# Kernel optimization log

Measured on AMD Instinct MI355X. Metric: run time of the kernel, lower is better.

The kernel has to match this reference:

```python
import jax, jax.numpy as jnp
from jax import lax
import numpy as np

B, H, W = 2, 48, 48
C_IN, C_OUT = 96, 192
D_INNER, N_STATE, DT_RANK, K = 192, 16, 6, 4  # VMamba: expand=2, d_state=16, dt_rank=ceil(C/16)
EPS = 1e-5


def setup_inputs() -> dict:
    ks = jax.random.split(jax.random.key(0), 16)
    s = 0.02
    r = lambda k, sh, sc=s: jax.random.normal(k, sh, jnp.float32) * sc
    d, N, R = D_INNER, N_STATE, DT_RANK
    return {
        "x": jax.random.normal(ks[0], (B, C_IN, H, W), jnp.float32),
        "ln_g": jnp.ones((C_IN,), jnp.float32),
        "ln_b": jnp.zeros((C_IN,), jnp.float32),
        "in_proj_w": r(ks[1], (2 * d, C_IN)),
        "dwconv_w": r(ks[2], (d, 1, 3, 3)),
        "dwconv_b": jnp.zeros((d,), jnp.float32),
        "x_proj_w": r(ks[3], (K, R + 2 * N, d)),
        "dt_w": r(ks[4], (K, d, R)),
        "dt_b": r(ks[5], (K, d), 0.1),
        "A_logs": jnp.tile(jnp.log(jnp.arange(1, N + 1, dtype=jnp.float32)), (K, d, 1)),
        "Ds": jnp.ones((K, d), jnp.float32),
        "out_norm_g": jnp.ones((d,), jnp.float32),
        "out_norm_b": jnp.zeros((d,), jnp.float32),
        "out_proj_w": r(ks[6], (C_IN, d)),
        "w1": r(ks[7], (C_OUT, C_IN, 1, 1)),
        "b1": jnp.zeros((C_OUT,), jnp.float32),
        "w31": r(ks[8], (C_OUT, C_IN, 3, 3)),
        "b31": jnp.zeros((C_OUT,), jnp.float32),
        "w32": r(ks[9], (C_OUT, C_IN, 3, 3)),
        "b32": jnp.zeros((C_OUT,), jnp.float32),
        "w33": r(ks[10], (C_OUT, C_OUT, 3, 3)),
        "b33": jnp.zeros((C_OUT,), jnp.float32),
        "bn_g": jnp.ones((3 * C_OUT,), jnp.float32),
        "bn_b": jnp.zeros((3 * C_OUT,), jnp.float32),
        "bn_m": r(ks[11], (3 * C_OUT,), 0.1),
        "bn_v": jax.random.uniform(ks[12], (3 * C_OUT,), jnp.float32) + 0.5,
        "prelu_a": jnp.float32(0.25),
    }


def _layernorm(x, g, b):
    m = jnp.mean(x, -1, keepdims=True)
    v = jnp.var(x, -1, keepdims=True)
    return (x - m) * lax.rsqrt(v + EPS) * g + b


def _conv(x, w, b, stride, pad, groups=1):
    y = lax.conv_general_dilated(x, w, (stride, stride), [(pad, pad), (pad, pad)],
                                 dimension_numbers=("NCHW", "OIHW", "NCHW"),
                                 feature_group_count=groups)
    return y + b[None, :, None, None]


def _ss2d(x, in_proj_w, dwconv_w, dwconv_b, x_proj_w, dt_w, dt_b, A_logs, Ds,
          out_norm_g, out_norm_b, out_proj_w):
    # x: (B, H, W, C)
    Bb, Hh, Ww, C = x.shape
    d, N, R = D_INNER, N_STATE, DT_RANK
    L = Hh * Ww
    xz = jnp.einsum("bhwc,ec->bhwe", x, in_proj_w)  # (B,H,W,2d)
    xin, z = jnp.split(xz, 2, axis=-1)
    xc = jnp.transpose(xin, (0, 3, 1, 2))           # (B,d,H,W)
    xc = jax.nn.silu(_conv(xc, dwconv_w, dwconv_b, 1, 1, groups=d))
    # 4 scan directions: row-major, col-major, and their reverses
    x_flat = xc.reshape(Bb, d, L)
    x_t = jnp.transpose(xc, (0, 1, 3, 2)).reshape(Bb, d, L)
    xs = jnp.stack([x_flat, x_t, x_flat[:, :, ::-1], x_t[:, :, ::-1]], axis=1)  # (B,K,d,L)
    x_dbl = jnp.einsum("bkdl,kcd->bkcl", xs, x_proj_w)
    dts, Bs, Cs = x_dbl[:, :, :R], x_dbl[:, :, R:R + N], x_dbl[:, :, R + N:]
    delta = jax.nn.softplus(jnp.einsum("bkrl,kdr->bkdl", dts, dt_w) + dt_b[None, :, :, None])
    A = -jnp.exp(A_logs)                                   # (K,d,N)
    dA = jnp.exp(jnp.einsum("bkdl,kdn->lbkdn", delta, A))  # (L,B,K,d,N)
    dBu = jnp.einsum("bkdl,bknl,bkdl->lbkdn", delta, Bs, xs)
    Cseq = jnp.transpose(Cs, (3, 0, 1, 2))                 # (L,B,K,N)

    def step(h, inp):
        dA_t, dBu_t, c_t = inp
        h = dA_t * h + dBu_t
        return h, jnp.einsum("bkdn,bkn->bkd", h, c_t)

    h0 = jnp.zeros((Bb, K, d, N), x.dtype)
    _, ys = lax.scan(step, h0, (dA, dBu, Cseq))            # ys: (L,B,K,d)
    ys = jnp.transpose(ys, (1, 2, 3, 0)) + xs * Ds[None, :, :, None]  # (B,K,d,L)

    def t_back(a):  # undo the HW transpose of col-major scans
        return jnp.transpose(a.reshape(Bb, d, Ww, Hh), (0, 1, 3, 2)).reshape(Bb, d, L)

    y = ys[:, 0] + ys[:, 2, :, ::-1] + t_back(ys[:, 1]) + t_back(ys[:, 3, :, ::-1])
    y = _layernorm(jnp.transpose(y, (0, 2, 1)), out_norm_g, out_norm_b).reshape(Bb, Hh, Ww, d)
    y = y * jax.nn.silu(z)
    return jnp.einsum("bhwd,cd->bhwc", y, out_proj_w)


def reference(x, ln_g, ln_b, in_proj_w, dwconv_w, dwconv_b, x_proj_w, dt_w, dt_b,
              A_logs, Ds, out_norm_g, out_norm_b, out_proj_w,
              w1, b1, w31, b31, w32, b32, w33, b33,
              bn_g, bn_b, bn_m, bn_v, prelu_a):
    # VSSBlock: residual + SS2D on LayerNorm'd NHWC features
    x_nhwc = jnp.transpose(x, (0, 2, 3, 1))
    x_nhwc = x_nhwc + _ss2d(_layernorm(x_nhwc, ln_g, ln_b), in_proj_w, dwconv_w,
                            dwconv_b, x_proj_w, dt_w, dt_b, A_logs, Ds,
                            out_norm_g, out_norm_b, out_proj_w)
    xm = jnp.transpose(x_nhwc, (0, 3, 1, 2))  # (B,C,H,W)
    # multi-branch stride-2 downsample
    x1 = _conv(xm, w1, b1, 2, 0)
    x2 = _conv(xm, w31, b31, 2, 1)
    x3 = _conv(_conv(xm, w32, b32, 2, 1), w33, b33, 1, 1)
    out = jnp.concatenate([x1, x2, x3], axis=1)  # (B, 3*C_OUT, H/2, W/2)
    # BatchNorm2d (inference, running stats) + PReLU(single param)
    out = (out - bn_m[None, :, None, None]) * lax.rsqrt(bn_v + EPS)[None, :, None, None] \
          * bn_g[None, :, None, None] + bn_b[None, :, None, None]
    return jnp.where(out > 0, out, prelu_a * out)
```

## Files before the change

kernel.cpp:

```cpp
#include <hip/hip_runtime.h>
#include <math.h>

#define BB_ 2
#define HH 48
#define WW 48
#define LL 2304
#define CIN 96
#define DD 192
#define KK 4
#define NN 16
#define RR 6
#define NCH 64
#define LC 36
#define COUT 192
#define OH 24
#define OW 24
#define OHW 576
#define NPX 1152
#define NTOT 4608
#define EPSF 1e-5f

__global__ __launch_bounds__(256) void k_prep(const float* __restrict__ x,
                                              const float* __restrict__ g,
                                              const float* __restrict__ b,
                                              const float* __restrict__ inw,
                                              const float* __restrict__ xpw,
                                              const float* __restrict__ w31,
                                              const float* __restrict__ w32,
                                              const float* __restrict__ w33,
                                              const float* __restrict__ w1,
                                              const float* __restrict__ wout,
                                              float* __restrict__ stats,
                                              float* __restrict__ WgT,
                                              float* __restrict__ sWg,
                                              float* __restrict__ sWb,
                                              float* __restrict__ At3,
                                              float* __restrict__ At1,
                                              float* __restrict__ At2,
                                              float* __restrict__ woutT) {
  __shared__ float tile[32][33];
  int bx = blockIdx.x;
  int tid = threadIdx.x;
  if (bx < 72) {
    int bb = bx / 36; int l0 = (bx % 36) * 64;
    int p = tid >> 2, q = tid & 3;
    int l = l0 + p;
    const float* xp = x + bb * CIN * LL + l;
    float s = 0.f, ss = 0.f;
    for (int c = q; c < CIN; c += 4) { float v = xp[c * LL]; s += v; ss += v * v; }
    s += __shfl_xor(s, 1, 64); s += __shfl_xor(s, 2, 64);
    ss += __shfl_xor(ss, 1, 64); ss += __shfl_xor(ss, 2, 64);
    if (q == 0) {
      float m = s / CIN; float var = ss / CIN - m * m;
      stats[(bb * LL + l) * 2 + 0] = m;
      stats[(bb * LL + l) * 2 + 1] = rsqrtf(var + EPSF);
    }
  } else if (bx == 72) {
    for (int e = tid; e < 2 * DD; e += 256) {
      float swg = 0.f, swb = 0.f;
      for (int c = 0; c < CIN; c++) {
        float w = inw[e * CIN + c];
        float wg = w * g[c];
        WgT[c * 384 + e] = wg;
        swg += wg; swb += w * b[c];
      }
      sWg[e] = swg; sWb[e] = swb;
    }
  } else if (bx < 218) {
    int idx = (bx - 73) * 256 + tid;
    if (idx < 192 * 192) {
      int m = idx % 192, d = idx / 192;
      At3[idx] = (m < 152) ? xpw[m * 192 + d] : 0.f;
    }
  } else if (bx < 542) {
    int tt = bx - 218;
    const float* srcw = (tt < 162) ? w31 : w32;
    int mofs = (tt < 162) ? 0 : 192;
    if (tt >= 162) tt -= 162;
    int kt = tt / 6, mt = tt % 6;
    int r = tid >> 5, c = tid & 31;
    for (int rr = r; rr < 32; rr += 8)
      tile[rr][c] = srcw[(mt * 32 + rr) * 864 + kt * 32 + c];
    __syncthreads();
    for (int rr = r; rr < 32; rr += 8)
      At1[(kt * 32 + rr) * 576 + mofs + mt * 32 + c] = tile[c][rr];
  } else if (bx < 1190) {
    int i = (bx - 542) * 256 + tid;
    if (i < 864 * 192) {
      int k = i / 192, m = i % 192;
      At1[k * 576 + 384 + m] = (k % 9 == 4) ? w1[m * 96 + k / 9] : 0.f;
    }
  } else if (bx < 1514) {
    int tt = bx - 1190;
    int kt = tt / 6, mt = tt % 6;
    int r = tid >> 5, c = tid & 31;
    for (int rr = r; rr < 32; rr += 8)
      tile[rr][c] = w33[(mt * 32 + rr) * 1728 + kt * 32 + c];
    __syncthreads();
    for (int rr = r; rr < 32; rr += 8)
      At2[(kt * 32 + rr) * 192 + mt * 32 + c] = tile[c][rr];
  } else {
    int i = (bx - 1514) * 256 + tid;
    if (i < 192 * 128) {
      int d = i / 128, e = i % 128;
      woutT[i] = (e < 96) ? wout[e * 192 + d] : 0.f;
    }
  }
}

__global__ __launch_bounds__(256) void k_dwconv(const float* __restrict__ xin,
                                                const float* __restrict__ wdw,
                                                const float* __restrict__ bdw,
                                                float* __restrict__ xs,
                                                float* __restrict__ xsl) {
  __shared__ float vt[32 * 50];
  int bid = blockIdx.x;
  int bb = bid / 288; int r = bid % 288; int dg = r / 72; int tile = r % 72;
  int l0 = tile * 32;
  int d0 = dg * 48;
  for (int i = threadIdx.x; i < 32 * 48; i += 256) {
    int lj = i & 31, dl = i >> 5;
    int d = d0 + dl;
    int l = l0 + lj;
    int h = l / WW, w = l % WW;
    const float* xp = xin + (bb * DD + d) * LL;
    const float* wq = wdw + d * 9;
    float acc = bdw[d];
#pragma unroll
    for (int kh = 0; kh < 3; kh++) {
      int ih = h + kh - 1; if (ih < 0 || ih >= HH) continue;
#pragma unroll
      for (int kw = 0; kw < 3; kw++) {
        int iw = w + kw - 1; if (iw < 0 || iw >= WW) continue;
        acc += xp[ih * WW + iw] * wq[kh * 3 + kw];
      }
    }
    float v = acc / (1.f + __expf(-acc));
    vt[lj * 50 + dl] = v;
    xsl[(size_t)d * NTOT + bb * LL + l] = v;
  }
  __syncthreads();
  for (int j = threadIdx.x; j < 32 * 48; j += 256) {
    int lj = j / 48, dl = j - lj * 48;
    int d = d0 + dl;
    int l = l0 + lj;
    int h = l / WW, w = l % WW;
    int lt = w * HH + h;
    float v = vt[lj * 50 + dl];
    xs[((size_t)(bb * 2 + 0) * LL + l) * DD + d] = v;
    xs[((size_t)(bb * 2 + 1) * LL + lt) * DD + d] = v;
  }
}

__global__ __launch_bounds__(256) void k_dtsplit(const float* __restrict__ C1,
                                                 const float* __restrict__ dtw,
                                                 const float* __restrict__ dtb,
                                                 float* __restrict__ Bsb,
                                                 float* __restrict__ Csb,
                                                 float* __restrict__ delta) {
  __shared__ float lds[38 * 33];
  int bid = blockIdx.x;
  int tile = bid % 72; int bk = bid / 72; int bb = bk >> 2; int k = bk & 3;
  int l0 = tile * 32;
  int tid = threadIdx.x;
  for (int i = tid; i < 38 * 32; i += 256) {
    int r = i >> 5, lj = i & 31;
    lds[r * 33 + lj] = C1[(size_t)(k * 38 + r) * NTOT + bb * LL + l0 + lj];
  }
  __syncthreads();
  for (int i = tid; i < 32 * 16; i += 256) {
    int lj = i >> 4, n = i & 15;
    int l = l0 + lj; int h = l / WW, w = l % WW; int lt = w * HH + h;
    int pos = (k == 0) ? l : (k == 1) ? lt : (k == 2) ? (LL - 1 - l) : (LL - 1 - lt);
    size_t base = ((size_t)bk * LL + pos) * NN + n;
    Bsb[base] = lds[(6 + n) * 33 + lj];
    Csb[base] = lds[(22 + n) * 33 + lj];
  }
  for (int i = tid; i < 32 * 192; i += 256) {
    int lj = i / 192, d = i - lj * 192;
    int l = l0 + lj; int h = l / WW, w = l % WW; int lt = w * HH + h;
    int pos = (k == 0) ? l : (k == 1) ? lt : (k == 2) ? (LL - 1 - l) : (LL - 1 - lt);
    const float* wd = dtw + (k * DD + d) * RR;
    float acc = dtb[k * DD + d];
#pragma unroll
    for (int r = 0; r < RR; r++) acc += wd[r] * lds[r * 33 + lj];
    float sp = acc > 20.f ? acc : log1pf(__expf(acc));
    delta[((size_t)bk * LL + pos) * DD + d] = sp;
  }
}

__global__ __launch_bounds__(192) void k_scan1(const float* __restrict__ delta,
                                               const float* __restrict__ xs,
                                               const float* __restrict__ Bsb,
                                               const float* __restrict__ A_logs,
                                               float* __restrict__ Pbuf,
                                               float* __restrict__ Sbuf) {
  __shared__ float Bls[LC * NN];
  int bid = blockIdx.x;
  int c = bid & (NCH - 1); int bk = bid >> 6; int k = bk & 3; int bb = bk >> 2;
  int t0 = c * LC;
  int d = threadIdx.x;
  const float* bp = Bsb + ((size_t)bk * LL + t0) * NN;
  for (int i = d; i < LC * NN; i += 192) Bls[i] = bp[i];
  float A[NN];
  {
    const float4* ap = (const float4*)(A_logs + (k * DD + d) * NN);
#pragma unroll
    for (int j = 0; j < 4; j++) {
      float4 a4 = ap[j];
      A[4 * j + 0] = -__expf(a4.x); A[4 * j + 1] = -__expf(a4.y);
      A[4 * j + 2] = -__expf(a4.z); A[4 * j + 3] = -__expf(a4.w);
    }
  }
  bool seq = true;
#pragma unroll
  for (int n = 0; n < NN; n++) seq = seq && (fabsf(A[n] + (float)(n + 1)) < 1e-3f);
  float h[NN];
#pragma unroll
  for (int n = 0; n < NN; n++) h[n] = 0.f;
  float sd = 0.f;
  __syncthreads();
  const float* dp = delta + ((size_t)bk * LL + t0) * DD + d;
  const float* xpb = xs + ((size_t)(bb * 2 + (k & 1)) * LL) * DD + d;
  const float* xp; int xstep;
  if (k < 2) { xp = xpb + (size_t)t0 * DD; xstep = DD; }
  else       { xp = xpb + (size_t)(LL - 1 - t0) * DD; xstep = -DD; }
#pragma unroll 2
  for (int t = 0; t < LC; ++t) {
    float dt = dp[t * DD];
    float xv = xp[t * xstep];
    float u = dt * xv;
    sd += dt;
    float dA[NN];
    if (seq) {
      float q = __expf(-dt);
      dA[0] = q;
#pragma unroll
      for (int n = 1; n < NN; n++) dA[n] = dA[n - 1] * q;
    } else {
#pragma unroll
      for (int n = 0; n < NN; n++) dA[n] = __expf(dt * A[n]);
    }
    const float4* b4 = (const float4*)&Bls[t * NN];
#pragma unroll
    for (int j = 0; j < 4; j++) {
      float4 bv = b4[j];
      h[4 * j + 0] = dA[4 * j + 0] * h[4 * j + 0] + u * bv.x;
      h[4 * j + 1] = dA[4 * j + 1] * h[4 * j + 1] + u * bv.y;
      h[4 * j + 2] = dA[4 * j + 2] * h[4 * j + 2] + u * bv.z;
      h[4 * j + 3] = dA[4 * j + 3] * h[4 * j + 3] + u * bv.w;
    }
  }
  int chn = (bk * DD + d) * NN;
  float* pp = Pbuf + (size_t)c * 24576 + chn;
  float* sp = Sbuf + (size_t)c * 24576 + chn;
#pragma unroll
  for (int n = 0; n < NN; n++) { pp[n] = __expf(A[n] * sd); sp[n] = h[n]; }
}

__global__ __launch_bounds__(256) void k_scan2(const float* __restrict__ Pbuf,
                                               const float* __restrict__ Sbuf,
                                               float* __restrict__ Hinit) {
  int idx = blockIdx.x * 256 + threadIdx.x;
  float h = 0.f;
  for (int c = 0; c < NCH; c++) {
    Hinit[(size_t)c * 24576 + idx] = h;
    h = Pbuf[(size_t)c * 24576 + idx] * h + Sbuf[(size_t)c * 24576 + idx];
  }
}

__global__ __launch_bounds__(192) void k_scan3(const float* __restrict__ delta,
                                               const float* __restrict__ xs,
                                               const float* __restrict__ Bsb,
                                               const float* __restrict__ Csb,
                                               const float* __restrict__ A_logs,
                                               const float* __restrict__ Ds,
                                               const float* __restrict__ Hinit,
                                               float* __restrict__ ys) {
  __shared__ float Bls[LC * NN];
  __shared__ float Cls[LC * NN];
  int bid = blockIdx.x;
  int c = bid & (NCH - 1); int bk = bid >> 6; int k = bk & 3; int bb = bk >> 2;
  int t0 = c * LC;
  int d = threadIdx.x;
  const float* bp = Bsb + ((size_t)bk * LL + t0) * NN;
  const float* cp = Csb + ((size_t)bk * LL + t0) * NN;
  for (int i = d; i < LC * NN; i += 192) { Bls[i] = bp[i]; Cls[i] = cp[i]; }
  float A[NN];
  {
    const float4* ap = (const float4*)(A_logs + (k * DD + d) * NN);
#pragma unroll
    for (int j = 0; j < 4; j++) {
      float4 a4 = ap[j];
      A[4 * j + 0] = -__expf(a4.x); A[4 * j + 1] = -__expf(a4.y);
      A[4 * j + 2] = -__expf(a4.z); A[4 * j + 3] = -__expf(a4.w);
    }
  }
  bool seq = true;
#pragma unroll
  for (int n = 0; n < NN; n++) seq = seq && (fabsf(A[n] + (float)(n + 1)) < 1e-3f);
  float Dv = Ds[k * DD + d];
  float h[NN];
  {
    const float4* hp = (const float4*)(Hinit + (size_t)c * 24576 + (bk * DD + d) * NN);
#pragma unroll
    for (int j = 0; j < 4; j++) {
      float4 h4 = hp[j];
      h[4 * j + 0] = h4.x; h[4 * j + 1] = h4.y;
      h[4 * j + 2] = h4.z; h[4 * j + 3] = h4.w;
    }
  }
  __syncthreads();
  const float* dp = delta + ((size_t)bk * LL + t0) * DD + d;
  const float* xpb = xs + ((size_t)(bb * 2 + (k & 1)) * LL) * DD + d;
  const float* xp; int xstep;
  if (k < 2) { xp = xpb + (size_t)t0 * DD; xstep = DD; }
  else       { xp = xpb + (size_t)(LL - 1 - t0) * DD; xstep = -DD; }
  float* yp = ys + ((size_t)bk * LL + t0) * DD + d;
#pragma unroll 2
  for (int t = 0; t < LC; ++t) {
    float dt = dp[t * DD];
    float xv = xp[t * xstep];
    float u = dt * xv;
    float y = 0.f;
    float dA[NN];
    if (seq) {
      float q = __expf(-dt);
      dA[0] = q;
#pragma unroll
      for (int n = 1; n < NN; n++) dA[n] = dA[n - 1] * q;
    } else {
#pragma unroll
      for (int n = 0; n < NN; n++) dA[n] = __expf(dt * A[n]);
    }
    const float4* b4 = (const float4*)&Bls[t * NN];
    const float4* c4 = (const float4*)&Cls[t * NN];
#pragma unroll
    for (int j = 0; j < 4; j++) {
      float4 bv = b4[j];
      float4 cc = c4[j];
      h[4 * j + 0] = dA[4 * j + 0] * h[4 * j + 0] + u * bv.x;
      h[4 * j + 1] = dA[4 * j + 1] * h[4 * j + 1] + u * bv.y;
      h[4 * j + 2] = dA[4 * j + 2] * h[4 * j + 2] + u * bv.z;
      h[4 * j + 3] = dA[4 * j + 3] * h[4 * j + 3] + u * bv.w;
      y += h[4 * j + 0] * cc.x + h[4 * j + 1] * cc.y
         + h[4 * j + 2] * cc.z + h[4 * j + 3] * cc.w;
    }
    yp[t * DD] = y + Dv * xv;
  }
}

__global__ __launch_bounds__(256) void k_combine(const float* __restrict__ ys,
                                                 const float* __restrict__ z,
                                                 const float* __restrict__ ong,
                                                 const float* __restrict__ onb,
                                                 float* __restrict__ ya) {
  __shared__ float yt[32 * 193];
  int bx = blockIdx.x; int bb = bx / 72; int l0 = (bx % 72) * 32;
  int tid = threadIdx.x;
  for (int i = tid; i < 32 * DD; i += 256) {
    int p = i / DD, d = i - p * DD;
    int l = l0 + p; int h = l / WW, w = l - h * WW;
    int t1 = w * HH + h;
    float v = ys[(((size_t)bb * KK + 0) * LL + l) * DD + d]
            + ys[(((size_t)bb * KK + 1) * LL + t1) * DD + d]
            + ys[(((size_t)bb * KK + 2) * LL + (LL - 1 - l)) * DD + d]
            + ys[(((size_t)bb * KK + 3) * LL + (LL - 1 - t1)) * DD + d];
    yt[p * 193 + d] = v;
  }
  __syncthreads();
  int p = tid >> 3, q = tid & 7;
  int l = l0 + p;
  float s = 0.f, ss = 0.f;
  for (int d = q * 24; d < q * 24 + 24; d++) { float v = yt[p * 193 + d]; s += v; ss += v * v; }
  s += __shfl_xor(s, 1, 64); s += __shfl_xor(s, 2, 64); s += __shfl_xor(s, 4, 64);
  ss += __shfl_xor(ss, 1, 64); ss += __shfl_xor(ss, 2, 64); ss += __shfl_xor(ss, 4, 64);
  float m = s / DD, var = ss / DD - m * m;
  float rr = rsqrtf(var + EPSF);
  const float* zp = z + (bb * LL + l) * DD;
  for (int d = q * 24; d < q * 24 + 24; d++) {
    float v = (yt[p * 193 + d] - m) * rr * ong[d] + onb[d];
    float zv = zp[d];
    yt[p * 193 + d] = v * zv / (1.f + __expf(-zv));
  }
  __syncthreads();
  for (int i = tid; i < 32 * DD; i += 256) {
    int d = i >> 5, p2 = i & 31;
    ya[(bb * DD + d) * LL + l0 + p2] = yt[p2 * 193 + d];
  }
}

template<int MT, int KCHUNK, int NB>
__global__ __launch_bounds__(256) void k_gemm(const float* __restrict__ At,
                                              const float* __restrict__ Bm,
                                              float* __restrict__ Cout) {
  __shared__ float As[16][64];
  __shared__ float Bs[16][64];
  int n0 = blockIdx.x * 64;
  int m0 = blockIdx.y * 64;
  int kz = blockIdx.z;
  int k0 = kz * KCHUNK;
  int tid = threadIdx.x;
  int lr = tid >> 4;
  int lc = (tid & 15) * 4;
  int tm = tid >> 4;
  int tn = tid & 15;
  float acc[4][4] = {};
  for (int ks = 0; ks < KCHUNK; ks += 16) {
    int kg = k0 + ks + lr;
    *(float4*)&As[lr][lc] = *(const float4*)&At[kg * MT + m0 + lc];
    *(float4*)&Bs[lr][lc] = *(const float4*)&Bm[(size_t)kg * NB + n0 + lc];
    __syncthreads();
#pragma unroll
    for (int kk = 0; kk < 16; kk++) {
      float4 a = *(float4*)&As[kk][tm * 4];
      float4 b = *(float4*)&Bs[kk][tn * 4];
      acc[0][0] += a.x * b.x; acc[0][1] += a.x * b.y; acc[0][2] += a.x * b.z; acc[0][3] += a.x * b.w;
      acc[1][0] += a.y * b.x; acc[1][1] += a.y * b.y; acc[1][2] += a.y * b.z; acc[1][3] += a.y * b.w;
      acc[2][0] += a.z * b.x; acc[2][1] += a.z * b.y; acc[2][2] += a.z * b.z; acc[2][3] += a.z * b.w;
      acc[3][0] += a.w * b.x; acc[3][1] += a.w * b.y; acc[3][2] += a.w * b.z; acc[3][3] += a.w * b.w;
    }
    __syncthreads();
  }
  float* cp = Cout + ((size_t)kz * MT + m0) * NB + n0;
#pragma unroll
  for (int i = 0; i < 4; i++) {
    float4 v = {acc[i][0], acc[i][1], acc[i][2], acc[i][3]};
    *(float4*)&cp[(size_t)(tm * 4 + i) * NB + tn * 4] = v;
  }
}

template<int MT, int KCHUNK, int CI, int IH, int STRIDE>
__global__ __launch_bounds__(256) void k_cgemm(const float* __restrict__ At,
                                               const float* __restrict__ SRC,
                                               float* __restrict__ Cout) {
  __shared__ float As[16][64];
  __shared__ float Bs[16][64];
  int n0 = blockIdx.x * 64;
  int m0 = blockIdx.y * 64;
  int kz = blockIdx.z;
  int k0 = kz * KCHUNK;
  int tid = threadIdx.x;
  int lr = tid >> 4;
  int lc = (tid & 15) * 4;
  int tm = tid >> 4;
  int tn = tid & 15;
  int n = n0 + lc;
  int bb = n / OHW;
  int rem = n - bb * OHW;
  int oh = rem / OW, ow0 = rem - oh * OW;
  float acc[4][4] = {};
  for (int ks = 0; ks < KCHUNK; ks += 16) {
    int kg = k0 + ks + lr;
    int ci = kg / 9, r9 = kg - ci * 9;
    int kh = r9 / 3, kw = r9 - kh * 3;
    int ih = STRIDE * oh + kh - 1;
    const float* src = SRC + ((size_t)(bb * CI + ci)) * (IH * IH) + ih * IH;
    float bvv[4];
#pragma unroll
    for (int j = 0; j < 4; j++) {
      int iw = STRIDE * (ow0 + j) + kw - 1;
      bvv[j] = (ih >= 0 && ih < IH && iw >= 0 && iw < IH) ? src[iw] : 0.f;
    }
    float4 bv = {bvv[0], bvv[1], bvv[2], bvv[3]};
    *(float4*)&Bs[lr][lc] = bv;
    *(float4*)&As[lr][lc] = *(const float4*)&At[kg * MT + m0 + lc];
    __syncthreads();
#pragma unroll
    for (int kk = 0; kk < 16; kk++) {
      float4 a = *(float4*)&As[kk][tm * 4];
      float4 b = *(float4*)&Bs[kk][tn * 4];
      acc[0][0] += a.x * b.x; acc[0][1] += a.x * b.y; acc[0][2] += a.x * b.z; acc[0][3] += a.x * b.w;
      acc[1][0] += a.y * b.x; acc[1][1] += a.y * b.y; acc[1][2] += a.y * b.z; acc[1][3] += a.y * b.w;
      acc[2][0] += a.z * b.x; acc[2][1] += a.z * b.y; acc[2][2] += a.z * b.z; acc[2][3] += a.z * b.w;
      acc[3][0] += a.w * b.x; acc[3][1] += a.w * b.y; acc[3][2] += a.w * b.z; acc[3][3] += a.w * b.w;
    }
    __syncthreads();
  }
  float* cp = Cout + ((size_t)kz * MT + m0) * NPX + n0;
#pragma unroll
  for (int i = 0; i < 4; i++) {
    float4 v = {acc[i][0], acc[i][1], acc[i][2], acc[i][3]};
    *(float4*)&cp[(size_t)(tm * 4 + i) * NPX + tn * 4] = v;
  }
}

template<int MT, int KD, int EPI>
__global__ __launch_bounds__(256) void k_gemmF(const float* __restrict__ At,
                                               const float* __restrict__ Bm,
                                               int ldb, int boffB,
                                               float* __restrict__ C0,
                                               int ldc, int boffC,
                                               const float* __restrict__ a0,
                                               const float* __restrict__ a1,
                                               const float* __restrict__ a2,
                                               float* __restrict__ a3) {
  __shared__ float As[16][64];
  __shared__ float Bs[16][64];
  int n0 = blockIdx.x * 64;
  int m0 = blockIdx.y * 64;
  int bb = blockIdx.z;
  const float* B = Bm + (size_t)bb * boffB;
  int tid = threadIdx.x;
  int lr = tid >> 4;
  int lc = (tid & 15) * 4;
  int tm = tid >> 4;
  int tn = tid & 15;
  float acc[4][4] = {};
  for (int ks = 0; ks < KD; ks += 16) {
    *(float4*)&As[lr][lc] = *(const float4*)&At[(ks + lr) * MT + m0 + lc];
    *(float4*)&Bs[lr][lc] = *(const float4*)&B[(size_t)(ks + lr) * ldb + n0 + lc];
    __syncthreads();
#pragma unroll
    for (int kk = 0; kk < 16; kk++) {
      float4 a = *(float4*)&As[kk][tm * 4];
      float4 b = *(float4*)&Bs[kk][tn * 4];
      acc[0][0] += a.x * b.x; acc[0][1] += a.x * b.y; acc[0][2] += a.x * b.z; acc[0][3] += a.x * b.w;
      acc[1][0] += a.y * b.x; acc[1][1] += a.y * b.y; acc[1][2] += a.y * b.z; acc[1][3] += a.y * b.w;
      acc[2][0] += a.z * b.x; acc[2][1] += a.z * b.y; acc[2][2] += a.z * b.z; acc[2][3] += a.z * b.w;
      acc[3][0] += a.w * b.x; acc[3][1] += a.w * b.y; acc[3][2] += a.w * b.z; acc[3][3] += a.w * b.w;
    }
    __syncthreads();
  }
  int n = n0 + tn * 4;
  if (EPI == 2) {
    float m_[4], r_[4];
#pragma unroll
    for (int j = 0; j < 4; j++) {
      m_[j] = a0[((size_t)bb * LL + n + j) * 2];
      r_[j] = a0[((size_t)bb * LL + n + j) * 2 + 1];
    }
#pragma unroll
    for (int i = 0; i < 4; i++) {
      int e = m0 + tm * 4 + i;
      float swg = a1[e], swb = a2[e];
      float v0 = r_[0] * (acc[i][0] - m_[0] * swg) + swb;
      float v1 = r_[1] * (acc[i][1] - m_[1] * swg) + swb;
      float v2 = r_[2] * (acc[i][2] - m_[2] * swg) + swb;
      float v3 = r_[3] * (acc[i][3] - m_[3] * swg) + swb;
      if (e < DD) {
        float4 v = {v0, v1, v2, v3};
        *(float4*)&C0[(size_t)bb * boffC + (size_t)e * ldc + n] = v;
      } else {
        a3[((size_t)bb * LL + n + 0) * DD + (e - DD)] = v0;
        a3[((size_t)bb * LL + n + 1) * DD + (e - DD)] = v1;
        a3[((size_t)bb * LL + n + 2) * DD + (e - DD)] = v2;
        a3[((size_t)bb * LL + n + 3) * DD + (e - DD)] = v3;
      }
    }
  } else {
#pragma unroll
    for (int i = 0; i < 4; i++) {
      int e = m0 + tm * 4 + i;
      if (e < CIN) {
        size_t off = (size_t)bb * boffC + (size_t)e * ldc + n;
        float4 xr = *(const float4*)&a0[off];
        float4 v = {acc[i][0] + xr.x, acc[i][1] + xr.y, acc[i][2] + xr.z, acc[i][3] + xr.w};
        *(float4*)&C0[off] = v;
      }
    }
  }
}

__global__ __launch_bounds__(256) void k_reduce1(const float* __restrict__ Cp1,
                                                 const float* __restrict__ b1,
                                                 const float* __restrict__ b31,
                                                 const float* __restrict__ b32,
                                                 const float* __restrict__ bn_g,
                                                 const float* __restrict__ bn_b,
                                                 const float* __restrict__ bn_m,
                                                 const float* __restrict__ bn_v,
                                                 const float* __restrict__ prelu_a,
                                                 float* __restrict__ out,
                                                 float* __restrict__ t3) {
  int idx = blockIdx.x * 256 + threadIdx.x;
  if (idx >= 576 * NPX) return;
  int m = idx / NPX, n = idx % NPX;
  float s = 0.f;
#pragma unroll
  for (int c = 0; c < 6; c++) s += Cp1[(size_t)c * 576 * NPX + idx];
  int bb = n / OHW, o = n % OHW;
  if (m < 192) {
    s += b31[m];
    int cc = 192 + m;
    float scale = rsqrtf(bn_v[cc] + EPSF) * bn_g[cc];
    float v = s * scale + (bn_b[cc] - bn_m[cc] * scale);
    float a = prelu_a[0];
    out[((size_t)bb * 576 + cc) * OHW + o] = v > 0.f ? v : a * v;
  } else if (m < 384) {
    s += b32[m - 192];
    t3[((size_t)bb * COUT + (m - 192)) * OHW + o] = s;
  } else {
    s += b1[m - 384];
    int cc = m - 384;
    float scale = rsqrtf(bn_v[cc] + EPSF) * bn_g[cc];
    float v = s * scale + (bn_b[cc] - bn_m[cc] * scale);
    float a = prelu_a[0];
    out[((size_t)bb * 576 + cc) * OHW + o] = v > 0.f ? v : a * v;
  }
}

__global__ __launch_bounds__(256) void k_reduce2(const float* __restrict__ Cp2,
                                                 const float* __restrict__ b33,
                                                 const float* __restrict__ bn_g,
                                                 const float* __restrict__ bn_b,
                                                 const float* __restrict__ bn_m,
                                                 const float* __restrict__ bn_v,
                                                 const float* __restrict__ prelu_a,
                                                 float* __restrict__ out) {
  int idx = blockIdx.x * 256 + threadIdx.x;
  if (idx >= 192 * NPX) return;
  int m = idx / NPX, n = idx % NPX;
  float s = b33[m];
#pragma unroll
  for (int c = 0; c < 9; c++) s += Cp2[(size_t)c * 192 * NPX + idx];
  int bb = n / OHW, o = n % OHW;
  int cc = 384 + m;
  float scale = rsqrtf(bn_v[cc] + EPSF) * bn_g[cc];
  float v = s * scale + (bn_b[cc] - bn_m[cc] * scale);
  float a = prelu_a[0];
  out[((size_t)bb * 576 + cc) * OHW + o] = v > 0.f ? v : a * v;
}

extern "C" void kernel_launch(void* const* d_in, const int* in_sizes, int n_in,
                              void* d_out, int out_size, void* d_ws, size_t ws_size,
                              hipStream_t stream) {
  const float* x        = (const float*)d_in[0];
  const float* ln_g     = (const float*)d_in[1];
  const float* ln_b     = (const float*)d_in[2];
  const float* in_proj_w= (const float*)d_in[3];
  const float* dwconv_w = (const float*)d_in[4];
  const float* dwconv_b = (const float*)d_in[5];
  const float* x_proj_w = (const float*)d_in[6];
  const float* dt_w     = (const float*)d_in[7];
  const float* dt_b     = (const float*)d_in[8];
  const float* A_logs   = (const float*)d_in[9];
  const float* Ds       = (const float*)d_in[10];
  const float* out_norm_g = (const float*)d_in[11];
  const float* out_norm_b = (const float*)d_in[12];
  const float* out_proj_w = (const float*)d_in[13];
  const float* w1  = (const float*)d_in[14];
  const float* b1  = (const float*)d_in[15];
  const float* w31 = (const float*)d_in[16];
  const float* b31 = (const float*)d_in[17];
  const float* w32 = (const float*)d_in[18];
  const float* b32 = (const float*)d_in[19];
  const float* w33 = (const float*)d_in[20];
  const float* b33 = (const float*)d_in[21];
  const float* bn_g = (const float*)d_in[22];
  const float* bn_b = (const float*)d_in[23];
  const float* bn_m = (const float*)d_in[24];
  const float* bn_v = (const float*)d_in[25];
  const float* prelu_a = (const float*)d_in[26];

  float* ws = (float*)d_ws;
  float* stats = ws + 0;
  float* WgT   = ws + 16384;
  float* sWg   = ws + 65536;
  float* sWb   = ws + 66048;
  float* At3   = ws + 98304;
  float* At1   = ws + 147456;
  float* At2   = ws + 655360;
  float* woutT = ws + 1048576;
  float* xin   = ws + 2097152;
  float* z     = ws + 3145728;
  float* xs    = ws + 4194304;
  float* xsl   = ws + 8388608;
  float* C1    = ws + 9437184;
  float* delta = ws + 10485760;
  float* Bsb   = ws + 14155776;
  float* Csb   = ws + 14680064;
  float* Pbuf  = ws + 15728640;
  float* Sbuf  = ws + 17301504;
  float* Hinit = ws + 18874368;
  float* ys    = ws + 20971520;
  float* ya    = ws + 25165824;
  float* xm    = ws + 26214400;
  float* t3    = ws + 27262976;
  float* Cp1   = ws + 31457280;
  float* Cp2   = ws + 35651584;
  float* out = (float*)d_out;

  k_prep<<<1610, 256, 0, stream>>>(x, ln_g, ln_b, in_proj_w, x_proj_w,
                                   w31, w32, w33, w1, out_proj_w,
                                   stats, WgT, sWg, sWb, At3, At1, At2, woutT);
  k_gemmF<384, 96, 2><<<dim3(36, 6, 2), 256, 0, stream>>>(
      WgT, x, LL, CIN * LL, xin, LL, DD * LL, stats, sWg, sWb, z);
  k_dwconv<<<576, 256, 0, stream>>>(xin, dwconv_w, dwconv_b, xs, xsl);
  k_gemm<192, 192, NTOT><<<dim3(72, 3, 1), 256, 0, stream>>>(At3, xsl, C1);
  k_dtsplit<<<576, 256, 0, stream>>>(C1, dt_w, dt_b, Bsb, Csb, delta);
  k_scan1<<<512, 192, 0, stream>>>(delta, xs, Bsb, A_logs, Pbuf, Sbuf);
  k_scan2<<<96, 256, 0, stream>>>(Pbuf, Sbuf, Hinit);
  k_scan3<<<512, 192, 0, stream>>>(delta, xs, Bsb, Csb, A_logs, Ds, Hinit, ys);
  k_combine<<<144, 256, 0, stream>>>(ys, z, out_norm_g, out_norm_b, ya);
  k_gemmF<128, 192, 3><<<dim3(36, 2, 2), 256, 0, stream>>>(
      woutT, ya, LL, DD * LL, xm, LL, CIN * LL, x, nullptr, nullptr, nullptr);
  k_cgemm<576, 144, CIN, HH, 2><<<dim3(18, 9, 6), 256, 0, stream>>>(At1, xm, Cp1);
  k_reduce1<<<2592, 256, 0, stream>>>(Cp1, b1, b31, b32, bn_g, bn_b, bn_m, bn_v,
                                      prelu_a, out, t3);
  k_cgemm<192, 192, COUT, OH, 1><<<dim3(18, 3, 9), 256, 0, stream>>>(At2, t3, Cp2);
  k_reduce2<<<864, 256, 0, stream>>>(Cp2, b33, bn_g, bn_b, bn_m, bn_v, prelu_a, out);
}
```

Before: 204.6 us.

## Use bf16 MFMA for conv GEMMs, fuse out_proj into combine, rechunk scan

The two implicit-GEMM convolution kernels now use bf16 MFMA 16x16x32 instructions in place of the fp32 FMA tiles, and the conv weights are converted to bf16 during prep. The output projection plus residual add is folded into the combine kernel using bf16 weights held in LDS, which removes the intermediate ya buffer and one GEMM launch. The scan chunk count goes from 64 to 96 and the dA power chain is computed by squaring to shorten the dependency chain. Using bf16 operands loses precision relative to fp32 and may push the result past the accuracy tolerance.

```diff
diff --git a/kernel.cpp b/kernel.cpp
--- a/kernel.cpp
+++ b/kernel.cpp
@@ -10,8 +10,8 @@
 #define KK 4
 #define NN 16
 #define RR 6
-#define NCH 64
-#define LC 36
+#define NCH 96
+#define LC 24
 #define COUT 192
 #define OH 24
 #define OW 24
@@ -19,6 +19,15 @@
 #define NPX 1152
 #define NTOT 4608
 #define EPSF 1e-5f
+
+typedef __attribute__((ext_vector_type(8))) short bf16x8;
+typedef __attribute__((ext_vector_type(4))) float f32x4;
+
+__device__ __forceinline__ short f2bf(float f) {
+  unsigned u = __float_as_uint(f);
+  unsigned r = (u + 0x7fffu + ((u >> 16) & 1u)) >> 16;
+  return (short)r;
+}
 
 __global__ __launch_bounds__(256) void k_prep(const float* __restrict__ x,
                                               const float* __restrict__ g,
@@ -35,10 +44,9 @@
                                               float* __restrict__ sWg,
                                               float* __restrict__ sWb,
                                               float* __restrict__ At3,
-                                              float* __restrict__ At1,
-                                              float* __restrict__ At2,
-                                              float* __restrict__ woutT) {
-  __shared__ float tile[32][33];
+                                              short* __restrict__ At1b,
+                                              short* __restrict__ At2b,
+                                              short* __restrict__ woutb) {
   int bx = blockIdx.x;
   int tid = threadIdx.x;
   if (bx < 72) {
@@ -66,45 +74,30 @@
       }
       sWg[e] = swg; sWb[e] = swb;
     }
-  } else if (bx < 218) {
+  } else if (bx < 217) {
     int idx = (bx - 73) * 256 + tid;
     if (idx < 192 * 192) {
       int m = idx % 192, d = idx / 192;
       At3[idx] = (m < 152) ? xpw[m * 192 + d] : 0.f;
     }
-  } else if (bx < 542) {
-    int tt = bx - 218;
-    const float* srcw = (tt < 162) ? w31 : w32;
-    int mofs = (tt < 162) ? 0 : 192;
-    if (tt >= 162) tt -= 162;
-    int kt = tt / 6, mt = tt % 6;
-    int r = tid >> 5, c = tid & 31;
-    for (int rr = r; rr < 32; rr += 8)
-      tile[rr][c] = srcw[(mt * 32 + rr) * 864 + kt * 32 + c];
-    __syncthreads();
-    for (int rr = r; rr < 32; rr += 8)
-      At1[(kt * 32 + rr) * 576 + mofs + mt * 32 + c] = tile[c][rr];
-  } else if (bx < 1190) {
-    int i = (bx - 542) * 256 + tid;
-    if (i < 864 * 192) {
-      int k = i / 192, m = i % 192;
-      At1[k * 576 + 384 + m] = (k % 9 == 4) ? w1[m * 96 + k / 9] : 0.f;
-    }
-  } else if (bx < 1514) {
-    int tt = bx - 1190;
-    int kt = tt / 6, mt = tt % 6;
-    int r = tid >> 5, c = tid & 31;
-    for (int rr = r; rr < 32; rr += 8)
-      tile[rr][c] = w33[(mt * 32 + rr) * 1728 + kt * 32 + c];
-    __syncthreads();
-    for (int rr = r; rr < 32; rr += 8)
-      At2[(kt * 32 + rr) * 192 + mt * 32 + c] = tile[c][rr];
+  } else if (bx < 2161) {
+    int i = (bx - 217) * 256 + tid;
+    if (i < 497664) {
+      float v;
+      if (i < 165888) v = w31[i];
+      else if (i < 331776) v = w32[i - 165888];
+      else {
+        int k = i % 864; int m = i / 864 - 384;
+        v = (k % 9 == 4) ? w1[m * 96 + k / 9] : 0.f;
+      }
+      At1b[i] = f2bf(v);
+    }
+  } else if (bx < 3457) {
+    int i = (bx - 2161) * 256 + tid;
+    if (i < 331776) At2b[i] = f2bf(w33[i]);
   } else {
-    int i = (bx - 1514) * 256 + tid;
-    if (i < 192 * 128) {
-      int d = i / 128, e = i % 128;
-      woutT[i] = (e < 96) ? wout[e * 192 + d] : 0.f;
-    }
+    int i = (bx - 3457) * 256 + tid;
+    if (i < 18432) woutb[i] = f2bf(wout[i]);
   }
 }
 
@@ -197,7 +190,7 @@
                                                float* __restrict__ Sbuf) {
   __shared__ float Bls[LC * NN];
   int bid = blockIdx.x;
-  int c = bid & (NCH - 1); int bk = bid >> 6; int k = bk & 3; int bb = bk >> 2;
+  int c = bid % NCH; int bk = bid / NCH; int k = bk & 3; int bb = bk >> 2;
   int t0 = c * LC;
   int d = threadIdx.x;
   const float* bp = Bsb + ((size_t)bk * LL + t0) * NN;
@@ -234,9 +227,11 @@
     float dA[NN];
     if (seq) {
       float q = __expf(-dt);
-      dA[0] = q;
-#pragma unroll
-      for (int n = 1; n < NN; n++) dA[n] = dA[n - 1] * q;
+      float q2 = q * q, q4 = q2 * q2, q8 = q4 * q4;
+      dA[0] = q; dA[1] = q2; dA[2] = q2 * q; dA[3] = q4;
+      dA[4] = q4 * q; dA[5] = q4 * q2; dA[6] = q4 * dA[2]; dA[7] = q8;
+      dA[8] = q8 * q; dA[9] = q8 * q2; dA[10] = q8 * dA[2]; dA[11] = q8 * q4;
+      dA[12] = q8 * dA[4]; dA[13] = q8 * dA[5]; dA[14] = q8 * dA[6]; dA[15] = q8 * q8;
     } else {
 #pragma unroll
       for (int n = 0; n < NN; n++) dA[n] = __expf(dt * A[n]);
@@ -280,7 +275,7 @@
   __shared__ float Bls[LC * NN];
   __shared__ float Cls[LC * NN];
   int bid = blockIdx.x;
-  int c = bid & (NCH - 1); int bk = bid >> 6; int k = bk & 3; int bb = bk >> 2;
+  int c = bid % NCH; int bk = bid / NCH; int k = bk & 3; int bb = bk >> 2;
   int t0 = c * LC;
   int d = threadIdx.x;
   const float* bp = Bsb + ((size_t)bk * LL + t0) * NN;
@@ -326,9 +321,11 @@
     float dA[NN];
     if (seq) {
       float q = __expf(-dt);
-      dA[0] = q;
-#pragma unroll
-      for (int n = 1; n < NN; n++) dA[n] = dA[n - 1] * q;
+      float q2 = q * q, q4 = q2 * q2, q8 = q4 * q4;
+      dA[0] = q; dA[1] = q2; dA[2] = q2 * q; dA[3] = q4;
+      dA[4] = q4 * q; dA[5] = q4 * q2; dA[6] = q4 * dA[2]; dA[7] = q8;
+      dA[8] = q8 * q; dA[9] = q8 * q2; dA[10] = q8 * dA[2]; dA[11] = q8 * q4;
+      dA[12] = q8 * dA[4]; dA[13] = q8 * dA[5]; dA[14] = q8 * dA[6]; dA[15] = q8 * q8;
     } else {
 #pragma unroll
       for (int n = 0; n < NN; n++) dA[n] = __expf(dt * A[n]);
@@ -350,14 +347,22 @@
   }
 }
 
-__global__ __launch_bounds__(256) void k_combine(const float* __restrict__ ys,
-                                                 const float* __restrict__ z,
-                                                 const float* __restrict__ ong,
-                                                 const float* __restrict__ onb,
-                                                 float* __restrict__ ya) {
-  __shared__ float yt[32 * 193];
+__global__ __launch_bounds__(256) void k_combineF(const float* __restrict__ ys,
+                                                  const float* __restrict__ z,
+                                                  const float* __restrict__ ong,
+                                                  const float* __restrict__ onb,
+                                                  const short* __restrict__ Wbf,
+                                                  const float* __restrict__ x,
+                                                  float* __restrict__ xm) {
+  __shared__ float yt[32 * 194];
+  __shared__ unsigned Wlu[96 * 98];
   int bx = blockIdx.x; int bb = bx / 72; int l0 = (bx % 72) * 32;
   int tid = threadIdx.x;
+  const unsigned* Wu = (const unsigned*)Wbf;
+  for (int i = tid; i < 96 * 96; i += 256) {
+    int e = i / 96, d2 = i - e * 96;
+    Wlu[e * 98 + d2] = Wu[i];
+  }
   for (int i = tid; i < 32 * DD; i += 256) {
     int p = i / DD, d = i - p * DD;
     int l = l0 + p; int h = l / WW, w = l - h * WW;
@@ -366,27 +371,42 @@
             + ys[(((size_t)bb * KK + 1) * LL + t1) * DD + d]
             + ys[(((size_t)bb * KK + 2) * LL + (LL - 1 - l)) * DD + d]
             + ys[(((size_t)bb * KK + 3) * LL + (LL - 1 - t1)) * DD + d];
-    yt[p * 193 + d] = v;
+    yt[p * 194 + d] = v;
   }
   __syncthreads();
   int p = tid >> 3, q = tid & 7;
   int l = l0 + p;
   float s = 0.f, ss = 0.f;
-  for (int d = q * 24; d < q * 24 + 24; d++) { float v = yt[p * 193 + d]; s += v; ss += v * v; }
+  for (int d = q * 24; d < q * 24 + 24; d++) { float v = yt[p * 194 + d]; s += v; ss += v * v; }
   s += __shfl_xor(s, 1, 64); s += __shfl_xor(s, 2, 64); s += __shfl_xor(s, 4, 64);
   ss += __shfl_xor(ss, 1, 64); ss += __shfl_xor(ss, 2, 64); ss += __shfl_xor(ss, 4, 64);
   float m = s / DD, var = ss / DD - m * m;
   float rr = rsqrtf(var + EPSF);
   const float* zp = z + (bb * LL + l) * DD;
   for (int d = q * 24; d < q * 24 + 24; d++) {
-    float v = (yt[p * 193 + d] - m) * rr * ong[d] + onb[d];
+    float v = (yt[p * 194 + d] - m) * rr * ong[d] + onb[d];
     float zv = zp[d];
-    yt[p * 193 + d] = v * zv / (1.f + __expf(-zv));
+    yt[p * 194 + d] = v * zv / (1.f + __expf(-zv));
   }
   __syncthreads();
-  for (int i = tid; i < 32 * DD; i += 256) {
-    int d = i >> 5, p2 = i & 31;
-    ya[(bb * DD + d) * LL + l0 + p2] = yt[p2 * 193 + d];
+  float acc[12];
+#pragma unroll
+  for (int j = 0; j < 12; j++) acc[j] = 0.f;
+  for (int d2 = 0; d2 < 96; d2++) {
+    float2 y2 = *(float2*)&yt[p * 194 + 2 * d2];
+#pragma unroll
+    for (int j = 0; j < 12; j++) {
+      unsigned wv = Wlu[(q * 12 + j) * 98 + d2];
+      float wlo = __uint_as_float(wv << 16);
+      float whi = __uint_as_float(wv & 0xffff0000u);
+      acc[j] += y2.x * wlo + y2.y * whi;
+    }
+  }
+#pragma unroll
+  for (int j = 0; j < 12; j++) {
+    int e = q * 12 + j;
+    size_t off = ((size_t)bb * CIN + e) * LL + l;
+    xm[off] = x[off] + acc[j];
   }
 }
 
@@ -430,62 +450,65 @@
   }
 }
 
-template<int MT, int KCHUNK, int CI, int IH, int STRIDE>
-__global__ __launch_bounds__(256) void k_cgemm(const float* __restrict__ At,
-                                               const float* __restrict__ SRC,
-                                               float* __restrict__ Cout) {
-  __shared__ float As[16][64];
-  __shared__ float Bs[16][64];
+template<int MT, int KTOT, int KCHUNK, int CI, int IH, int STRIDE>
+__global__ __launch_bounds__(256) void k_cgemm_mfma(const short* __restrict__ Abf,
+                                                    const float* __restrict__ SRC,
+                                                    float* __restrict__ Cout) {
+  __shared__ short As[64][40];
+  __shared__ short Bs[64][40];
   int n0 = blockIdx.x * 64;
   int m0 = blockIdx.y * 64;
   int kz = blockIdx.z;
   int k0 = kz * KCHUNK;
   int tid = threadIdx.x;
-  int lr = tid >> 4;
-  int lc = (tid & 15) * 4;
-  int tm = tid >> 4;
-  int tn = tid & 15;
-  int n = n0 + lc;
-  int bb = n / OHW;
-  int rem = n - bb * OHW;
-  int oh = rem / OW, ow0 = rem - oh * OW;
-  float acc[4][4] = {};
-  for (int ks = 0; ks < KCHUNK; ks += 16) {
-    int kg = k0 + ks + lr;
-    int ci = kg / 9, r9 = kg - ci * 9;
-    int kh = r9 / 3, kw = r9 - kh * 3;
-    int ih = STRIDE * oh + kh - 1;
-    const float* src = SRC + ((size_t)(bb * CI + ci)) * (IH * IH) + ih * IH;
-    float bvv[4];
-#pragma unroll
-    for (int j = 0; j < 4; j++) {
-      int iw = STRIDE * (ow0 + j) + kw - 1;
-      bvv[j] = (ih >= 0 && ih < IH && iw >= 0 && iw < IH) ? src[iw] : 0.f;
-    }
-    float4 bv = {bvv[0], bvv[1], bvv[2], bvv[3]};
-    *(float4*)&Bs[lr][lc] = bv;
-    *(float4*)&As[lr][lc] = *(const float4*)&At[kg * MT + m0 + lc];
+  int lane = tid & 63;
+  int wv = tid >> 6;
+  int row16 = lane & 15;
+  int kg = lane >> 4;
+  int sm = tid >> 2;
+  int sk8 = (tid & 3) * 8;
+  int n = n0 + sm;
+  int bb = n / OHW; int rem = n - bb * OHW;
+  int oh = rem / OW, ow = rem - oh * OW;
+  f32x4 acc[4];
+#pragma unroll
+  for (int i = 0; i < 4; i++) acc[i] = (f32x4){0.f, 0.f, 0.f, 0.f};
+  for (int ks = 0; ks < KCHUNK; ks += 32) {
+    *(bf16x8*)&As[sm][sk8] =
+        *(const bf16x8*)&Abf[(size_t)(m0 + sm) * KTOT + k0 + ks + sk8];
+    bf16x8 bvv;
+#pragma unroll
+    for (int j = 0; j < 8; j++) {
+      int k = k0 + ks + sk8 + j;
+      int ci = k / 9; int r9 = k - ci * 9;
+      int kh = r9 / 3, kw = r9 - kh * 3;
+      int ih = STRIDE * oh + kh - 1;
+      int iw = STRIDE * ow + kw - 1;
+      float v = (ih >= 0 && ih < IH && iw >= 0 && iw < IH)
+              ? SRC[((size_t)(bb * CI + ci) * IH + ih) * IH + iw] : 0.f;
+      bvv[j] = f2bf(v);
+    }
+    *(bf16x8*)&Bs[sm][sk8] = bvv;
     __syncthreads();
-#pragma unroll
-    for (int kk = 0; kk < 16; kk++) {
-      float4 a = *(float4*)&As[kk][tm * 4];
-      float4 b = *(float4*)&Bs[kk][tn * 4];
-      acc[0][0] += a.x * b.x; acc[0][1] += a.x * b.y; acc[0][2] += a.x * b.z; acc[0][3] += a.x * b.w;
-      acc[1][0] += a.y * b.x; acc[1][1] += a.y * b.y; acc[1][2] += a.y * b.z; acc[1][3] += a.y * b.w;
-      acc[2][0] += a.z * b.x; acc[2][1] += a.z * b.y; acc[2][2] += a.z * b.z; acc[2][3] += a.z * b.w;
-      acc[3][0] += a.w * b.x; acc[3][1] += a.w * b.y; acc[3][2] += a.w * b.z; acc[3][3] += a.w * b.w;
+    bf16x8 a = *(const bf16x8*)&As[wv * 16 + row16][kg * 8];
+#pragma unroll
+    for (int tn = 0; tn < 4; tn++) {
+      bf16x8 b = *(const bf16x8*)&Bs[tn * 16 + row16][kg * 8];
+      acc[tn] = __builtin_amdgcn_mfma_f32_16x16x32_bf16(a, b, acc[tn], 0, 0, 0);
     }
     __syncthreads();
   }
-  float* cp = Cout + ((size_t)kz * MT + m0) * NPX + n0;
-#pragma unroll
-  for (int i = 0; i < 4; i++) {
-    float4 v = {acc[i][0], acc[i][1], acc[i][2], acc[i][3]};
-    *(float4*)&cp[(size_t)(tm * 4 + i) * NPX + tn * 4] = v;
-  }
-}
-
-template<int MT, int KD, int EPI>
+#pragma unroll
+  for (int tn = 0; tn < 4; tn++) {
+    int col = n0 + tn * 16 + row16;
+    int rowb = m0 + wv * 16 + kg * 4;
+#pragma unroll
+    for (int i = 0; i < 4; i++)
+      Cout[((size_t)kz * MT + rowb + i) * NPX + col] = acc[tn][i];
+  }
+}
+
+template<int MT, int KD>
 __global__ __launch_bounds__(256) void k_gemmF(const float* __restrict__ At,
                                                const float* __restrict__ Bm,
                                                int ldb, int boffB,
@@ -523,41 +546,28 @@
     __syncthreads();
   }
   int n = n0 + tn * 4;
-  if (EPI == 2) {
-    float m_[4], r_[4];
-#pragma unroll
-    for (int j = 0; j < 4; j++) {
-      m_[j] = a0[((size_t)bb * LL + n + j) * 2];
-      r_[j] = a0[((size_t)bb * LL + n + j) * 2 + 1];
-    }
-#pragma unroll
-    for (int i = 0; i < 4; i++) {
-      int e = m0 + tm * 4 + i;
-      float swg = a1[e], swb = a2[e];
-      float v0 = r_[0] * (acc[i][0] - m_[0] * swg) + swb;
-      float v1 = r_[1] * (acc[i][1] - m_[1] * swg) + swb;
-      float v2 = r_[2] * (acc[i][2] - m_[2] * swg) + swb;
-      float v3 = r_[3] * (acc[i][3] - m_[3] * swg) + swb;
-      if (e < DD) {
-        float4 v = {v0, v1, v2, v3};
-        *(float4*)&C0[(size_t)bb * boffC + (size_t)e * ldc + n] = v;
-      } else {
-        a3[((size_t)bb * LL + n + 0) * DD + (e - DD)] = v0;
-        a3[((size_t)bb * LL + n + 1) * DD + (e - DD)] = v1;
-        a3[((size_t)bb * LL + n + 2) * DD + (e - DD)] = v2;
-        a3[((size_t)bb * LL + n + 3) * DD + (e - DD)] = v3;
-      }
-    }
-  } else {
-#pragma unroll
-    for (int i = 0; i < 4; i++) {
-      int e = m0 + tm * 4 + i;
-      if (e < CIN) {
-        size_t off = (size_t)bb * boffC + (size_t)e * ldc + n;
-        float4 xr = *(const float4*)&a0[off];
-        float4 v = {acc[i][0] + xr.x, acc[i][1] + xr.y, acc[i][2] + xr.z, acc[i][3] + xr.w};
-        *(float4*)&C0[off] = v;
-      }
+  float m_[4], r_[4];
+#pragma unroll
+  for (int j = 0; j < 4; j++) {
+    m_[j] = a0[((size_t)bb * LL + n + j) * 2];
+    r_[j] = a0[((size_t)bb * LL + n + j) * 2 + 1];
+  }
+#pragma unroll
+  for (int i = 0; i < 4; i++) {
+    int e = m0 + tm * 4 + i;
+    float swg = a1[e], swb = a2[e];
+    float v0 = r_[0] * (acc[i][0] - m_[0] * swg) + swb;
+    float v1 = r_[1] * (acc[i][1] - m_[1] * swg) + swb;
+    float v2 = r_[2] * (acc[i][2] - m_[2] * swg) + swb;
+    float v3 = r_[3] * (acc[i][3] - m_[3] * swg) + swb;
+    if (e < DD) {
+      float4 v = {v0, v1, v2, v3};
+      *(float4*)&C0[(size_t)bb * boffC + (size_t)e * ldc + n] = v;
+    } else {
+      a3[((size_t)bb * LL + n + 0) * DD + (e - DD)] = v0;
+      a3[((size_t)bb * LL + n + 1) * DD + (e - DD)] = v1;
+      a3[((size_t)bb * LL + n + 2) * DD + (e - DD)] = v2;
+      a3[((size_t)bb * LL + n + 3) * DD + (e - DD)] = v3;
     }
   }
 }
@@ -578,7 +588,7 @@
   int m = idx / NPX, n = idx % NPX;
   float s = 0.f;
 #pragma unroll
-  for (int c = 0; c < 6; c++) s += Cp1[(size_t)c * 576 * NPX + idx];
+  for (int c = 0; c < 9; c++) s += Cp1[(size_t)c * 576 * NPX + idx];
   int bb = n / OHW, o = n % OHW;
   if (m < 192) {
     s += b31[m];
@@ -659,9 +669,9 @@
   float* sWg   = ws + 65536;
   float* sWb   = ws + 66048;
   float* At3   = ws + 98304;
-  float* At1   = ws + 147456;
-  float* At2   = ws + 655360;
-  float* woutT = ws + 1048576;
+  short* At1b  = (short*)(ws + 147456);
+  short* At2b  = (short*)(ws + 397312);
+  short* woutb = (short*)(ws + 565248);
   float* xin   = ws + 2097152;
   float* z     = ws + 3145728;
   float* xs    = ws + 4194304;
@@ -671,33 +681,32 @@
   float* Bsb   = ws + 14155776;
   float* Csb   = ws + 14680064;
   float* Pbuf  = ws + 15728640;
-  float* Sbuf  = ws + 17301504;
-  float* Hinit = ws + 18874368;
-  float* ys    = ws + 20971520;
-  float* ya    = ws + 25165824;
-  float* xm    = ws + 26214400;
-  float* t3    = ws + 27262976;
+  float* Sbuf  = ws + 18874368;
+  float* Hinit = ws + 22020096;
+  float* ys    = ws + 25165824;
+  float* xm    = ws + 29360128;
+  float* t3    = ws + 30408704;
   float* Cp1   = ws + 31457280;
-  float* Cp2   = ws + 35651584;
+  float* Cp2   = ws + 37748736;
   float* out = (float*)d_out;
 
-  k_prep<<<1610, 256, 0, stream>>>(x, ln_g, ln_b, in_proj_w, x_proj_w,
+  k_prep<<<3529, 256, 0, stream>>>(x, ln_g, ln_b, in_proj_w, x_proj_w,
                                    w31, w32, w33, w1, out_proj_w,
-                                   stats, WgT, sWg, sWb, At3, At1, At2, woutT);
-  k_gemmF<384, 96, 2><<<dim3(36, 6, 2), 256, 0, stream>>>(
+                                   stats, WgT, sWg, sWb, At3, At1b, At2b, woutb);
+  k_gemmF<384, 96><<<dim3(36, 6, 2), 256, 0, stream>>>(
       WgT, x, LL, CIN * LL, xin, LL, DD * LL, stats, sWg, sWb, z);
   k_dwconv<<<576, 256, 0, stream>>>(xin, dwconv_w, dwconv_b, xs, xsl);
   k_gemm<192, 192, NTOT><<<dim3(72, 3, 1), 256, 0, stream>>>(At3, xsl, C1);
   k_dtsplit<<<576, 256, 0, stream>>>(C1, dt_w, dt_b, Bsb, Csb, delta);
-  k_scan1<<<512, 192, 0, stream>>>(delta, xs, Bsb, A_logs, Pbuf, Sbuf);
+  k_scan1<<<768, 192, 0, stream>>>(delta, xs, Bsb, A_logs, Pbuf, Sbuf);
   k_scan2<<<96, 256, 0, stream>>>(Pbuf, Sbuf, Hinit);
-  k_scan3<<<512, 192, 0, stream>>>(delta, xs, Bsb, Csb, A_logs, Ds, Hinit, ys);
-  k_combine<<<144, 256, 0, stream>>>(ys, z, out_norm_g, out_norm_b, ya);
-  k_gemmF<128, 192, 3><<<dim3(36, 2, 2), 256, 0, stream>>>(
-      woutT, ya, LL, DD * LL, xm, LL, CIN * LL, x, nullptr, nullptr, nullptr);
-  k_cgemm<576, 144, CIN, HH, 2><<<dim3(18, 9, 6), 256, 0, stream>>>(At1, xm, Cp1);
+  k_scan3<<<768, 192, 0, stream>>>(delta, xs, Bsb, Csb, A_logs, Ds, Hinit, ys);
+  k_combineF<<<144, 256, 0, stream>>>(ys, z, out_norm_g, out_norm_b, woutb, x, xm);
+  k_cgemm_mfma<576, 864, 96, CIN, HH, 2><<<dim3(18, 9, 9), 256, 0, stream>>>(
+      At1b, xm, Cp1);
   k_reduce1<<<2592, 256, 0, stream>>>(Cp1, b1, b31, b32, bn_g, bn_b, bn_m, bn_v,
                                       prelu_a, out, t3);
-  k_cgemm<192, 192, COUT, OH, 1><<<dim3(18, 3, 9), 256, 0, stream>>>(At2, t3, Cp2);
+  k_cgemm_mfma<192, 1728, 192, COUT, OH, 1><<<dim3(18, 3, 9), 256, 0, stream>>>(
+      At2b, t3, Cp2);
   k_reduce2<<<864, 256, 0, stream>>>(Cp2, b33, bn_g, bn_b, bn_m, bn_v, prelu_a, out);
 }
```

Measured after the change: 186.8 us. 8.7% less time.
